# Performance work log

Measured on AMD Instinct MI355X. Metric: run time of the kernel, lower is better.

Reference implementation:

```python
import jax, jax.numpy as jnp
from jax import lax
import numpy as np

# ---- geometry constants (from metadata / module __init__) ----
NA = 1152            # rotview (number of projection angles)
ND = 736             # det_count
NP = 512             # reconstructed image size
VOX = 1.0 / 0.7      # vox_scaling
D   = VOX * 595.0    # source-to-isocenter distance
DD  = VOX * 490.6    # isocenter-to-detector distance
DU  = VOX * 1.2858   # detector pixel spacing
DSD = D + DD         # source-to-detector distance
ANGLES = np.linspace(0.0, 2.0 * np.pi, NA, endpoint=False) + np.pi / 2.0

# ---- Shepp-Logan Fourier filter (skimage/torch-radon construction) ----
PAD = max(64, int(2 ** np.ceil(np.log2(2 * ND))))  # 2048

def _shepp_logan_filter(size):
    n = np.concatenate([np.arange(1, size // 2 + 1, 2),
                        np.arange(size // 2 - 1, 0, -2)])
    f = np.zeros(size)
    f[0] = 0.25
    f[1::2] = -1.0 / (np.pi * n) ** 2
    four = 2.0 * np.real(np.fft.fft(f))            # ramp filter
    omega = np.pi * np.fft.fftfreq(size)[1:]
    four[1:] *= np.sin(omega) / omega              # Shepp-Logan window
    return four[: size // 2 + 1].astype(np.float32)  # rfft half-spectrum

FILT = jnp.asarray(_shepp_logan_filter(PAD))
COS_A = jnp.asarray(np.cos(ANGLES).astype(np.float32))
SIN_A = jnp.asarray(np.sin(ANGLES).astype(np.float32))


def _filter_sinogram(sino):
    # sino: (NA, ND). Zero-pad to PAD, filter in Fourier domain, crop.
    padded = jnp.pad(sino, ((0, 0), (0, PAD - ND)))
    spec = jnp.fft.rfft(padded, axis=-1) * FILT
    filt = jnp.fft.irfft(spec, n=PAD, axis=-1)[:, :ND]
    return filt * (np.pi / (2.0 * NA))


def _backproject(filtered):
    # Pixel-driven fan-beam (flat detector) backprojection.
    c = (NP - 1) / 2.0
    coords = jnp.arange(NP, dtype=jnp.float32) - c
    ys, xs = jnp.meshgrid(coords, coords, indexing='ij')  # (NP, NP)

    def body(acc, inp):
        cb, sb, row = inp
        pdot = xs * cb + ys * sb            # pixel coord along source dir
        pe = -xs * sb + ys * cb             # pixel coord along detector axis
        den = D - pdot                      # source->pixel depth
        u = DSD * pe / den                  # detector coordinate (mm)
        iu = u / DU + (ND - 1) / 2.0        # fractional detector index
        i0 = jnp.floor(iu)
        frac = iu - i0
        i0i = i0.astype(jnp.int32)
        valid = (i0i >= 0) & (i0i < ND - 1) & (den > 0)
        i0c = jnp.clip(i0i, 0, ND - 2)
        v = row[i0c] * (1.0 - frac) + row[i0c + 1] * frac  # linear interp
        w = (D / den) ** 2                   # fan-beam distance weighting
        return acc + jnp.where(valid, w * v, 0.0), None

    img, _ = lax.scan(body, jnp.zeros((NP, NP), jnp.float32),
                      (COS_A, SIN_A, filtered))
    return img


def setup_inputs() -> dict:
    key = jax.random.key(0)
    x = jax.random.normal(key, (1, 1, NA, ND), dtype=jnp.float32)
    return {"x": x}


def reference(x):
    sino = x[0, 0]                          # (NA, ND) after squeeze
    filtered = _filter_sinogram(sino)
    fbp = _backproject(filtered)
    # mu -> HU -> normalize to [0, 1] window
    fbp_hu = (1000.0 * ((fbp - 0.0192) / 0.0192) - (-1024.0)) / (3072.0 - (-1024.0))
    return fbp_hu[None, None]               # (1, 1, 512, 512)
```

## Files before the change

### kernel.cpp

```cpp
#include <hip/hip_runtime.h>
#include <math.h>

#ifndef M_PI
#define M_PI 3.14159265358979323846
#endif

#define NAANG 1152
#define NDET  736
#define NPIX  512
#define PADN  2048
#define NHALF 1025

#define OFF_COST  0
#define OFF_FILTF 8192
#define OFF_H     12416
#define OFF_TRIG  20608
#define OFF_FS    39040
#define OFF_PART  3430528

typedef int int32x4_t __attribute__((ext_vector_type(4)));
typedef float f32x2 __attribute__((ext_vector_type(2)));
__device__ f32x2 llvm_amdgcn_struct_buffer_load_2xfp32(int32x4_t srsrc,
                                                       int vindex, int voffset,
                                                       int soffset, int cachepolicy)
    __asm("llvm.amdgcn.struct.buffer.load.v2f32");

__global__ void costab_kernel(float* __restrict__ cosT) {
    int r = blockIdx.x * 256 + threadIdx.x;
    cosT[r] = (float)cos(2.0 * M_PI * (double)r / (double)PADN);
}

__global__ void filt_spec_kernel(const float* __restrict__ cosT,
                                 float* __restrict__ filt_f) {
    __shared__ float red[256];
    const int m = blockIdx.x;
    const int t = threadIdx.x;
    float s = 0.f;
    for (int j = t; j < 1024; j += 256) {
        int n = (j < 512) ? (2 * j + 1) : (2047 - 2 * j);
        float fj = (float)(-1.0 / ((M_PI * n) * (M_PI * n)));
        s += fj * cosT[(m * (2 * j + 1)) & (PADN - 1)];
    }
    red[t] = s;
    __syncthreads();
    for (int w = 128; w > 0; w >>= 1) {
        if (t < w) red[t] += red[t + w];
        __syncthreads();
    }
    if (t == 0) {
        double four = 2.0 * (0.25 + (double)red[0]);
        if (m > 0) {
            double om = M_PI * (double)m / (double)PADN;
            four *= sin(om) / om;
        }
        filt_f[m] = (float)four;
    }
}

__global__ void h_kernel(const float* __restrict__ cosT,
                         const float* __restrict__ filt_f,
                         float* __restrict__ h, float4* __restrict__ trig) {
    __shared__ float red[256];
    const int k = blockIdx.x;
    const int t = threadIdx.x;
    if (t == 0 && k < NAANG) {
        double ang = 2.0 * M_PI * (double)k / (double)NAANG + M_PI / 2.0;
        double c = cos(ang), s = sin(ang);
        double K = 1085.6 / 1.2858;
        trig[k] = make_float4((float)c, (float)s, (float)(K * c), (float)(K * s));
    }
    float s = 0.f;
    for (int m = t; m <= 1024; m += 256) {
        float F = filt_f[m];
        float c;
        if (m == 0) c = 1.f;
        else if (m == 1024) c = (k & 1) ? -1.f : 1.f;
        else c = 2.f * cosT[(m * k) & (PADN - 1)];
        s += F * c;
    }
    red[t] = s;
    __syncthreads();
    for (int w = 128; w > 0; w >>= 1) {
        if (t < w) red[t] += red[t + w];
        __syncthreads();
    }
    if (t == 0)
        h[k] = (float)((double)red[0] / (double)PADN * (M_PI / (2.0 * (double)NAANG)));
}

__global__ void conv_kernel(const float* __restrict__ x,
                            const float* __restrict__ h,
                            float* __restrict__ fs) {
    __shared__ float sh2[2816];
    __shared__ float srow[NDET];
    const int row = blockIdx.x;
    const int t = threadIdx.x;
    const float4* h4 = (const float4*)h;
    for (int i = t; i < 704; i += 192) ((float4*)sh2)[i] = h4[i & 511];
    const float4* x4 = (const float4*)(x + row * NDET);
    for (int i = t; i < NDET / 4; i += 192) ((float4*)srow)[i] = x4[i];
    __syncthreads();

    const int t4 = 4 * t;
    float o0 = 0.f, o1 = 0.f, o2 = 0.f, o3 = 0.f;
    #pragma unroll 2
    for (int j = 0; j < NDET; j += 4) {
        float4 r4 = *(const float4*)&srow[j];
        const int A = t4 + PADN - j;
        float4 hlo = *(const float4*)&sh2[A - 4];
        float4 hhi = *(const float4*)&sh2[A];
        o0 = fmaf(r4.x, hhi.x, o0); o0 = fmaf(r4.y, hlo.w, o0);
        o0 = fmaf(r4.z, hlo.z, o0); o0 = fmaf(r4.w, hlo.y, o0);
        o1 = fmaf(r4.x, hhi.y, o1); o1 = fmaf(r4.y, hhi.x, o1);
        o1 = fmaf(r4.z, hlo.w, o1); o1 = fmaf(r4.w, hlo.z, o1);
        o2 = fmaf(r4.x, hhi.z, o2); o2 = fmaf(r4.y, hhi.y, o2);
        o2 = fmaf(r4.z, hhi.x, o2); o2 = fmaf(r4.w, hlo.w, o2);
        o3 = fmaf(r4.x, hhi.w, o3); o3 = fmaf(r4.y, hhi.z, o3);
        o3 = fmaf(r4.z, hhi.y, o3); o3 = fmaf(r4.w, hhi.x, o3);
    }
    if (t < NDET / 4)
        *(float4*)&fs[row * NDET + t4] = make_float4(o0, o1, o2, o3);
}

#define GEO(AA, S)                                                       \
  {                                                                      \
    float4 q = trig[abase + (AA)];           \
    const float* rp_ = fs + (size_t)(abase + (AA)) * NDET;               \
    uintptr_t ua_ = (uintptr_t)rp_;                                      \
    int32x4_t sA_ = { (int)ua_, (int)(ua_ >> 32) | 0x00040000, 736,      \
                      0x00020000 };                                      \
    float den0 = fmaf(-xs, q.x, fmaf(-ys0, q.y, Dg));                    \
    float kpe0 = fmaf(ys0, q.z, -(xs * q.w));                            \
    float den1 = den0 - q.y, den2 = den1 - q.y, den3 = den2 - q.y;       \
    float kpe1 = kpe0 + q.z, kpe2 = kpe1 + q.z, kpe3 = kpe2 + q.z;       \
    float r0 = __builtin_amdgcn_rcpf(den0);                              \
    float r1 = __builtin_amdgcn_rcpf(den1);                              \
    float r2 = __builtin_amdgcn_rcpf(den2);                              \
    float r3 = __builtin_amdgcn_rcpf(den3);                              \
    float iu0 = fmaf(kpe0, r0, 367.5f);                                  \
    float iu1 = fmaf(kpe1, r1, 367.5f);                                  \
    float iu2 = fmaf(kpe2, r2, 367.5f);                                  \
    float iu3 = fmaf(kpe3, r3, 367.5f);                                  \
    int i0 = (int)floorf(iu0);                                           \
    int i1 = (int)floorf(iu1);                                           \
    int i2 = (int)floorf(iu2);                                           \
    int i3 = (int)floorf(iu3);                                           \
    asm("v_fract_f32 %0, %1" : "=v"(S##f0) : "v"(iu0));                  \
    asm("v_fract_f32 %0, %1" : "=v"(S##f1) : "v"(iu1));                  \
    asm("v_fract_f32 %0, %1" : "=v"(S##f2) : "v"(iu2));                  \
    asm("v_fract_f32 %0, %1" : "=v"(S##f3) : "v"(iu3));                  \
    S##g0 = llvm_amdgcn_struct_buffer_load_2xfp32(sA_, i0, 0, 0, 0);     \
    S##g1 = llvm_amdgcn_struct_buffer_load_2xfp32(sA_, i1, 0, 0, 0);     \
    S##g2 = llvm_amdgcn_struct_buffer_load_2xfp32(sA_, i2, 0, 0, 0);     \
    S##g3 = llvm_amdgcn_struct_buffer_load_2xfp32(sA_, i3, 0, 0, 0);     \
    float w0_ = r0 * r0, w1_ = r1 * r1, w2_ = r2 * r2, w3_ = r3 * r3;    \
    S##w0 = (iu0 < 735.0f) ? w0_ : 0.f;                                  \
    S##w1 = (iu1 < 735.0f) ? w1_ : 0.f;                                  \
    S##w2 = (iu2 < 735.0f) ? w2_ : 0.f;                                  \
    S##w3 = (iu3 < 735.0f) ? w3_ : 0.f;                                  \
  }

#define CONSUME(S)                                                       \
  {                                                                      \
    float v0 = fmaf(S##f0, S##g0.y - S##g0.x, S##g0.x);                  \
    float v1 = fmaf(S##f1, S##g1.y - S##g1.x, S##g1.x);                  \
    float v2 = fmaf(S##f2, S##g2.y - S##g2.x, S##g2.x);                  \
    float v3 = fmaf(S##f3, S##g3.y - S##g3.x, S##g3.x);                  \
    acc0 = fmaf(S##w0, v0, acc0); acc1 = fmaf(S##w1, v1, acc1);          \
    acc2 = fmaf(S##w2, v2, acc2); acc3 = fmaf(S##w3, v3, acc3);          \
  }

#define DECLSET(S)                                                       \
    f32x2 S##g0, S##g1, S##g2, S##g3;                                    \
    float S##f0, S##f1, S##f2, S##f3, S##w0, S##w1, S##w2, S##w3;

template<int NCH>
__global__ __launch_bounds__(256, 8)
void backproj_kernel(const float* __restrict__ fs,
                     const float4* __restrict__ trig,
                     float* __restrict__ partial) {
    constexpr int ACL = NAANG / NCH;
    const int t = threadIdx.x;
    const int abase = blockIdx.z * ACL;
    const int ix = blockIdx.x * 256 + t;
    const int iy = blockIdx.y * 4;
    const float xs  = (float)ix - 255.5f;
    const float ys0 = (float)iy - 255.5f;
    const float Dg = 850.0f;

    float acc0 = 0.f, acc1 = 0.f, acc2 = 0.f, acc3 = 0.f;
    DECLSET(A) DECLSET(B)

    GEO(0, A);
    int a = 0;
    for (; a + 2 < ACL; a += 2) {
        GEO(a + 1, B); CONSUME(A);
        GEO(a + 2, A); CONSUME(B);
    }
    GEO(ACL - 1, B);
    CONSUME(A); CONSUME(B);

    float* outp = partial + ((size_t)blockIdx.z * NPIX + iy) * NPIX + ix;
    outp[0 * NPIX] = acc0;
    outp[1 * NPIX] = acc1;
    outp[2 * NPIX] = acc2;
    outp[3 * NPIX] = acc3;
}

template<int NCH>
__global__ void combine_kernel(const float* __restrict__ partial,
                               float* __restrict__ out) {
    int p = blockIdx.x * 256 + threadIdx.x;
    float s = 0.f;
    #pragma unroll
    for (int c = 0; c < NCH; ++c) s += partial[c * NPIX * NPIX + p];
    out[p] = fmaf(s, (float)(722500.0 * 1000.0 / 0.0192 / 4096.0), 0.005859375f);
}

extern "C" void kernel_launch(void* const* d_in, const int* in_sizes, int n_in,
                              void* d_out, int out_size, void* d_ws, size_t ws_size,
                              hipStream_t stream) {
    const float* x = (const float*)d_in[0];
    float* out = (float*)d_out;

    char* ws = (char*)d_ws;
    float*  cosT   = (float*)(ws + OFF_COST);
    float*  filt_f = (float*)(ws + OFF_FILTF);
    float*  h      = (float*)(ws + OFF_H);
    float4* trig   = (float4*)(ws + OFF_TRIG);
    float*  fs     = (float*)(ws + OFF_FS);
    float*  part   = (float*)(ws + OFF_PART);

    costab_kernel<<<PADN / 256, 256, 0, stream>>>(cosT);
    filt_spec_kernel<<<NHALF, 256, 0, stream>>>(cosT, filt_f);
    h_kernel<<<PADN, 256, 0, stream>>>(cosT, filt_f, h, trig);
    conv_kernel<<<NAANG, 192, 0, stream>>>(x, h, fs);

    const size_t pbytes = (size_t)NPIX * NPIX * 4;
    if (ws_size >= OFF_PART + 8 * pbytes) {
        backproj_kernel<8><<<dim3(2, 128, 8), 256, 0, stream>>>(fs, trig, part);
        combine_kernel<8><<<NPIX * NPIX / 256, 256, 0, stream>>>(part, out);
    } else if (ws_size >= OFF_PART + 4 * pbytes) {
        backproj_kernel<4><<<dim3(2, 128, 4), 256, 0, stream>>>(fs, trig, part);
        combine_kernel<4><<<NPIX * NPIX / 256, 256, 0, stream>>>(part, out);
    } else if (ws_size >= OFF_PART + 2 * pbytes) {
        backproj_kernel<2><<<dim3(2, 128, 2), 256, 0, stream>>>(fs, trig, part);
        combine_kernel<2><<<NPIX * NPIX / 256, 256, 0, stream>>>(part, out);
    } else {
        backproj_kernel<1><<<dim3(2, 128, 1), 256, 0, stream>>>(fs, trig, part);
        combine_kernel<1><<<NPIX * NPIX / 256, 256, 0, stream>>>(part, out);
    }
}
```

Before: 262.8 us.

## Stage filtered sinogram rows in double-buffered LDS for backprojection gathers

Replaces the per-pixel raw buffer loads from global memory with a block-wide staging of each angle's filtered detector row into shared memory. The row is double-buffered so the next angle's row is fetched while the current one is consumed. The gathers then become LDS reads with clamped indices, and the bounds check moves to an unsigned index comparison. In exchange, every angle now needs a __syncthreads, the software pipelining across two angles is dropped, and the extra LDS use may lower occupancy.

```diff
diff --git a/kernel.cpp b/kernel.cpp
--- a/kernel.cpp
+++ b/kernel.cpp
@@ -17,13 +17,6 @@
 #define OFF_TRIG  20608
 #define OFF_FS    39040
 #define OFF_PART  3430528
-
-typedef int int32x4_t __attribute__((ext_vector_type(4)));
-typedef float f32x2 __attribute__((ext_vector_type(2)));
-__device__ f32x2 llvm_amdgcn_struct_buffer_load_2xfp32(int32x4_t srsrc,
-                                                       int vindex, int voffset,
-                                                       int soffset, int cachepolicy)
-    __asm("llvm.amdgcn.struct.buffer.load.v2f32");
 
 __global__ void costab_kernel(float* __restrict__ cosT) {
     int r = blockIdx.x * 256 + threadIdx.x;
@@ -122,64 +115,13 @@
         *(float4*)&fs[row * NDET + t4] = make_float4(o0, o1, o2, o3);
 }
 
-#define GEO(AA, S)                                                       \
-  {                                                                      \
-    float4 q = trig[abase + (AA)];           \
-    const float* rp_ = fs + (size_t)(abase + (AA)) * NDET;               \
-    uintptr_t ua_ = (uintptr_t)rp_;                                      \
-    int32x4_t sA_ = { (int)ua_, (int)(ua_ >> 32) | 0x00040000, 736,      \
-                      0x00020000 };                                      \
-    float den0 = fmaf(-xs, q.x, fmaf(-ys0, q.y, Dg));                    \
-    float kpe0 = fmaf(ys0, q.z, -(xs * q.w));                            \
-    float den1 = den0 - q.y, den2 = den1 - q.y, den3 = den2 - q.y;       \
-    float kpe1 = kpe0 + q.z, kpe2 = kpe1 + q.z, kpe3 = kpe2 + q.z;       \
-    float r0 = __builtin_amdgcn_rcpf(den0);                              \
-    float r1 = __builtin_amdgcn_rcpf(den1);                              \
-    float r2 = __builtin_amdgcn_rcpf(den2);                              \
-    float r3 = __builtin_amdgcn_rcpf(den3);                              \
-    float iu0 = fmaf(kpe0, r0, 367.5f);                                  \
-    float iu1 = fmaf(kpe1, r1, 367.5f);                                  \
-    float iu2 = fmaf(kpe2, r2, 367.5f);                                  \
-    float iu3 = fmaf(kpe3, r3, 367.5f);                                  \
-    int i0 = (int)floorf(iu0);                                           \
-    int i1 = (int)floorf(iu1);                                           \
-    int i2 = (int)floorf(iu2);                                           \
-    int i3 = (int)floorf(iu3);                                           \
-    asm("v_fract_f32 %0, %1" : "=v"(S##f0) : "v"(iu0));                  \
-    asm("v_fract_f32 %0, %1" : "=v"(S##f1) : "v"(iu1));                  \
-    asm("v_fract_f32 %0, %1" : "=v"(S##f2) : "v"(iu2));                  \
-    asm("v_fract_f32 %0, %1" : "=v"(S##f3) : "v"(iu3));                  \
-    S##g0 = llvm_amdgcn_struct_buffer_load_2xfp32(sA_, i0, 0, 0, 0);     \
-    S##g1 = llvm_amdgcn_struct_buffer_load_2xfp32(sA_, i1, 0, 0, 0);     \
-    S##g2 = llvm_amdgcn_struct_buffer_load_2xfp32(sA_, i2, 0, 0, 0);     \
-    S##g3 = llvm_amdgcn_struct_buffer_load_2xfp32(sA_, i3, 0, 0, 0);     \
-    float w0_ = r0 * r0, w1_ = r1 * r1, w2_ = r2 * r2, w3_ = r3 * r3;    \
-    S##w0 = (iu0 < 735.0f) ? w0_ : 0.f;                                  \
-    S##w1 = (iu1 < 735.0f) ? w1_ : 0.f;                                  \
-    S##w2 = (iu2 < 735.0f) ? w2_ : 0.f;                                  \
-    S##w3 = (iu3 < 735.0f) ? w3_ : 0.f;                                  \
-  }
-
-#define CONSUME(S)                                                       \
-  {                                                                      \
-    float v0 = fmaf(S##f0, S##g0.y - S##g0.x, S##g0.x);                  \
-    float v1 = fmaf(S##f1, S##g1.y - S##g1.x, S##g1.x);                  \
-    float v2 = fmaf(S##f2, S##g2.y - S##g2.x, S##g2.x);                  \
-    float v3 = fmaf(S##f3, S##g3.y - S##g3.x, S##g3.x);                  \
-    acc0 = fmaf(S##w0, v0, acc0); acc1 = fmaf(S##w1, v1, acc1);          \
-    acc2 = fmaf(S##w2, v2, acc2); acc3 = fmaf(S##w3, v3, acc3);          \
-  }
-
-#define DECLSET(S)                                                       \
-    f32x2 S##g0, S##g1, S##g2, S##g3;                                    \
-    float S##f0, S##f1, S##f2, S##f3, S##w0, S##w1, S##w2, S##w3;
-
 template<int NCH>
 __global__ __launch_bounds__(256, 8)
 void backproj_kernel(const float* __restrict__ fs,
                      const float4* __restrict__ trig,
                      float* __restrict__ partial) {
     constexpr int ACL = NAANG / NCH;
+    __shared__ float row2[2][768];
     const int t = threadIdx.x;
     const int abase = blockIdx.z * ACL;
     const int ix = blockIdx.x * 256 + t;
@@ -189,16 +131,70 @@
     const float Dg = 850.0f;
 
     float acc0 = 0.f, acc1 = 0.f, acc2 = 0.f, acc3 = 0.f;
-    DECLSET(A) DECLSET(B)
-
-    GEO(0, A);
-    int a = 0;
-    for (; a + 2 < ACL; a += 2) {
-        GEO(a + 1, B); CONSUME(A);
-        GEO(a + 2, A); CONSUME(B);
-    }
-    GEO(ACL - 1, B);
-    CONSUME(A); CONSUME(B);
+
+    if (t < 184) {
+        float4 v = ((const float4*)(fs + (size_t)abase * NDET))[t];
+        ((float4*)&row2[0][0])[t] = v;
+    }
+    __syncthreads();
+
+    int cur = 0;
+    #pragma unroll 2
+    for (int a = 0; a < ACL; ++a) {
+        float4 nv;
+        const bool stager = (t < 184) && (a + 1 < ACL);
+        if (stager)
+            nv = ((const float4*)(fs + (size_t)(abase + a + 1) * NDET))[t];
+
+        float4 q = trig[abase + a];
+        const float* row = &row2[cur][0];
+        float den0 = fmaf(-xs, q.x, fmaf(-ys0, q.y, Dg));
+        float kpe0 = fmaf(ys0, q.z, -(xs * q.w));
+        float den1 = den0 - q.y, den2 = den1 - q.y, den3 = den2 - q.y;
+        float kpe1 = kpe0 + q.z, kpe2 = kpe1 + q.z, kpe3 = kpe2 + q.z;
+        float r0 = __builtin_amdgcn_rcpf(den0);
+        float r1 = __builtin_amdgcn_rcpf(den1);
+        float r2 = __builtin_amdgcn_rcpf(den2);
+        float r3 = __builtin_amdgcn_rcpf(den3);
+        float iu0 = fmaf(kpe0, r0, 367.5f);
+        float iu1 = fmaf(kpe1, r1, 367.5f);
+        float iu2 = fmaf(kpe2, r2, 367.5f);
+        float iu3 = fmaf(kpe3, r3, 367.5f);
+        int i0 = (int)floorf(iu0);
+        int i1 = (int)floorf(iu1);
+        int i2 = (int)floorf(iu2);
+        int i3 = (int)floorf(iu3);
+        float fr0, fr1, fr2, fr3;
+        asm("v_fract_f32 %0, %1" : "=v"(fr0) : "v"(iu0));
+        asm("v_fract_f32 %0, %1" : "=v"(fr1) : "v"(iu1));
+        asm("v_fract_f32 %0, %1" : "=v"(fr2) : "v"(iu2));
+        asm("v_fract_f32 %0, %1" : "=v"(fr3) : "v"(iu3));
+        int c0 = min(max(i0, 0), NDET - 2);
+        int c1 = min(max(i1, 0), NDET - 2);
+        int c2 = min(max(i2, 0), NDET - 2);
+        int c3 = min(max(i3, 0), NDET - 2);
+        float a0 = row[c0], b0 = row[c0 + 1];
+        float a1 = row[c1], b1 = row[c1 + 1];
+        float a2 = row[c2], b2 = row[c2 + 1];
+        float a3 = row[c3], b3 = row[c3 + 1];
+        float w0 = ((unsigned)i0 < (unsigned)(NDET - 1)) ? r0 * r0 : 0.f;
+        float w1 = ((unsigned)i1 < (unsigned)(NDET - 1)) ? r1 * r1 : 0.f;
+        float w2 = ((unsigned)i2 < (unsigned)(NDET - 1)) ? r2 * r2 : 0.f;
+        float w3 = ((unsigned)i3 < (unsigned)(NDET - 1)) ? r3 * r3 : 0.f;
+        float v0 = fmaf(fr0, b0 - a0, a0);
+        float v1 = fmaf(fr1, b1 - a1, a1);
+        float v2 = fmaf(fr2, b2 - a2, a2);
+        float v3 = fmaf(fr3, b3 - a3, a3);
+        acc0 = fmaf(w0, v0, acc0);
+        acc1 = fmaf(w1, v1, acc1);
+        acc2 = fmaf(w2, v2, acc2);
+        acc3 = fmaf(w3, v3, acc3);
+
+        if (stager)
+            ((float4*)&row2[cur ^ 1][0])[t] = nv;
+        __syncthreads();
+        cur ^= 1;
+    }
 
     float* outp = partial + ((size_t)blockIdx.z * NPIX + iy) * NPIX + ix;
     outp[0 * NPIX] = acc0;
```

Measured after the change: 275.7 us. 4.9% more time.
